# Performance work log

Measured on AMD Instinct MI355X. Metric: run time of the kernel, lower is better.

The kernel has to match this reference:

```python
import jax, jax.numpy as jnp
import numpy as np

N = 50000   # nodes
E = 800000  # edges (avg degree 16)
D = 96      # input feature dim
U = 96      # units (== D, so no dense_i projection)


def _glorot(key, fan_in, fan_out):
    limit = np.sqrt(6.0 / (fan_in + fan_out)).astype(np.float32)
    return jax.random.uniform(key, (fan_in, fan_out), jnp.float32, -limit, limit)


def setup_inputs() -> dict:
    key = jax.random.key(0)
    ks = jax.random.split(key, 8)
    X = jax.random.normal(ks[0], (N, D), jnp.float32)
    row = jax.random.randint(ks[1], (E,), 0, N, jnp.int32)   # destination nodes
    col = jax.random.randint(ks[2], (E,), 0, N, jnp.int32)   # source nodes
    a_vals = jax.random.uniform(ks[3], (E,), jnp.float32)    # adjacency values
    return {
        "X": X,
        "a_vals": a_vals,
        "Wn": _glorot(ks[4], D, U), "bn": jnp.zeros((U,), jnp.float32),
        "Wgi": _glorot(ks[5], D, U), "bgi": jnp.zeros((U,), jnp.float32),
        "Wgn": _glorot(ks[6], U, U), "bgn": jnp.zeros((U,), jnp.float32),
        "row": row, "col": col,
    }


def reference(X, a_vals, Wn, bn, Wgi, bgi, Wgn, bgn, row, col):
    # new_X = dense_n(X); new_X = A @ new_X  (SpMM via gather + segment_sum)
    newX = X @ Wn + bn                       # [N, U]
    msgs = a_vals[:, None] * newX[col]       # [E, U]
    agg = jax.ops.segment_sum(msgs, row, num_segments=N)  # [N, U]
    # gate = sigmoid(dense_gate_i(X) + dense_gate_n(agg))
    gate = jax.nn.sigmoid(X @ Wgi + bgi + agg @ Wgn + bgn)
    # units == inp_dim -> no dense_i; gated residual combine
    return agg * gate + X * (1.0 - gate)
```

## Files before the change

kernel.cpp:

```cpp
#include <hip/hip_runtime.h>
#include <math.h>


#define DU 96
#define DU4 24
#define NSUB 32
#define NGRP 8
#define HMAX 6656
#define CAPG_PAD 16384

typedef unsigned int uint;
typedef unsigned short ushort;
typedef __attribute__((ext_vector_type(8))) short short8;
typedef __attribute__((ext_vector_type(4))) float f32x4;

__device__ inline uint bf16r(float x) {
  uint u = __float_as_uint(x);
  return (u + 0x7FFFu + ((u >> 16) & 1u)) >> 16;
}

__global__ __launch_bounds__(256) void k_fuse1(
    const float* __restrict__ X, const float* __restrict__ Wn,
    const float* __restrict__ bn, const float* __restrict__ Wgi,
    const float* __restrict__ Wgn, const int* __restrict__ row,
    ushort* __restrict__ Xb, ushort* __restrict__ newXb,
    ushort* __restrict__ WTgi, ushort* __restrict__ WTgn,
    ushort* __restrict__ pc, int N, int E, int ntile) {
  __shared__ __align__(16) char smem[31744];
  ushort* WL = (ushort*)smem;
  typedef ushort XsRow[104];
  XsRow* Xs = (XsRow*)(smem + 18432);
  const int tid = threadIdx.x;
  const int lane = tid & 63, w = tid >> 6;
  const int m = lane & 15, q = lane >> 4;

  if ((int)blockIdx.x < ntile) {
    if (blockIdx.x == 0) {
      for (int i = tid; i < DU * DU; i += 256) {
        int n = i / DU, k = i % DU;
        WTgi[i] = (ushort)bf16r(Wgi[k * DU + n]);
      }
    } else if (blockIdx.x == 1) {
      for (int i = tid; i < DU * DU; i += 256) {
        int n = i / DU, k = i % DU;
        WTgn[i] = (ushort)bf16r(Wgn[k * DU + n]);
      }
    }
    for (int idx = tid; idx < 9216; idx += 256) {
      int j = idx & 7, ln = (idx >> 3) & 63, tk = idx >> 9;
      int ks = tk / 6, t = tk % 6;
      int k = ks * 32 + (ln >> 4) * 8 + j;
      int n = t * 16 + (ln & 15);
      WL[idx] = (ushort)bf16r(Wn[k * DU + n]);
    }
    const int row0 = blockIdx.x * 64;
    for (int i = tid; i < 64 * 48; i += 256) {
      int r = i / 48, cu = i % 48;
      int gr = row0 + r;
      uint packed = 0;
      if (gr < N) {
        float2 v = ((const float2*)X)[(size_t)gr * 48 + cu];
        packed = bf16r(v.x) | (bf16r(v.y) << 16);
        ((uint*)Xb)[(size_t)gr * 48 + cu] = packed;
      }
      *(uint*)&Xs[r][cu * 2] = packed;
    }
    __syncthreads();

    f32x4 acc[6];
#pragma unroll
    for (int t = 0; t < 6; ++t) acc[t] = (f32x4){0.f, 0.f, 0.f, 0.f};
#pragma unroll
    for (int ks = 0; ks < 3; ++ks) {
      short8 af = *(const short8*)&Xs[w * 16 + m][ks * 32 + q * 8];
#pragma unroll
      for (int t = 0; t < 6; ++t) {
        short8 bf = *(const short8*)&WL[((ks * 6 + t) * 64 + lane) * 8];
        acc[t] = __builtin_amdgcn_mfma_f32_16x16x32_bf16(af, bf, acc[t], 0, 0, 0);
      }
    }
    __syncthreads();
#pragma unroll
    for (int t = 0; t < 6; ++t) {
      int c = t * 16 + m;
      float bb = bn[c];
#pragma unroll
      for (int i = 0; i < 4; ++i)
        Xs[w * 16 + q * 4 + i][c] = (ushort)bf16r(acc[t][i] + bb);
    }
    __syncthreads();
    for (int i = tid; i < 64 * 48; i += 256) {
      int r = i / 48, cu = i % 48;
      int gr = row0 + r;
      if (gr < N) ((uint*)newXb)[(size_t)gr * 48 + cu] = *(uint*)&Xs[r][cu * 2];
    }
  } else {
    int* hist = (int*)smem;
    const int hb = (int)blockIdx.x - ntile;
    const int g = (int)(blockIdx.x & 7);
    const int sub = hb >> 3;
    const int d0 = (int)((long long)N * g >> 3);
    const int d1 = (int)((long long)N * (g + 1) >> 3);
    const int hs = d1 - d0;
    for (int j = tid; j < hs; j += 256) hist[j] = 0;
    __syncthreads();
    const int e0 = (int)(((long long)E * sub) / NSUB);
    const int e1 = (int)(((long long)E * (sub + 1)) / NSUB);
    int i = e0 + tid;
    for (; i + 1792 < e1; i += 2048) {
      int a0 = row[i], a1 = row[i + 256], a2 = row[i + 512], a3 = row[i + 768];
      int a4 = row[i + 1024], a5 = row[i + 1280], a6 = row[i + 1536], a7 = row[i + 1792];
      if (a0 >= d0 && a0 < d1) atomicAdd(&hist[a0 - d0], 1);
      if (a1 >= d0 && a1 < d1) atomicAdd(&hist[a1 - d0], 1);
      if (a2 >= d0 && a2 < d1) atomicAdd(&hist[a2 - d0], 1);
      if (a3 >= d0 && a3 < d1) atomicAdd(&hist[a3 - d0], 1);
      if (a4 >= d0 && a4 < d1) atomicAdd(&hist[a4 - d0], 1);
      if (a5 >= d0 && a5 < d1) atomicAdd(&hist[a5 - d0], 1);
      if (a6 >= d0 && a6 < d1) atomicAdd(&hist[a6 - d0], 1);
      if (a7 >= d0 && a7 < d1) atomicAdd(&hist[a7 - d0], 1);
    }
    for (; i < e1; i += 256) {
      int d = row[i];
      if (d >= d0 && d < d1) atomicAdd(&hist[d - d0], 1);
    }
    __syncthreads();
    for (int j = tid; j < hs; j += 256) pc[(size_t)sub * N + d0 + j] = (ushort)hist[j];
  }
}

__global__ __launch_bounds__(1024) void k_prep(const ushort* __restrict__ pc,
                                               ushort* __restrict__ psub,
                                               ushort* __restrict__ deg,
                                               int* __restrict__ off,
                                               int N, int E) {
  __shared__ ushort degs[HMAX];
  __shared__ int ws[16];
  const int g = blockIdx.x;
  const int tid = threadIdx.x;
  const int lane = tid & 63, wid = tid >> 6;
  const int d0 = (int)((long long)N * g >> 3);
  const int d1 = (int)((long long)N * (g + 1) >> 3);
  const int hs = d1 - d0;
  for (int j2 = tid * 2; j2 < hs; j2 += 2048) {
    int d2 = d0 + j2;
    int runLo = 0, runHi = 0;
#pragma unroll 8
    for (int s = 0; s < NSUB; ++s) {
      uint v = *(const uint*)(pc + (size_t)s * N + d2);
      *(uint*)(psub + (size_t)s * N + d2) = (uint)runLo | ((uint)runHi << 16);
      runLo += (int)(v & 0xFFFFu);
      runHi += (int)(v >> 16);
    }
    uint dpair = (uint)runLo | ((uint)runHi << 16);
    *(uint*)&degs[j2] = dpair;
    *(uint*)(deg + d2) = dpair;
  }
  __syncthreads();
  const int PT = 8;
  const int j0 = tid * PT;
  int v[PT];
  int s = 0;
#pragma unroll
  for (int k = 0; k < PT; ++k) {
    int j = j0 + k;
    v[k] = (j < hs) ? (int)degs[j] : 0;
    s += v[k];
  }
  int incl = s;
#pragma unroll
  for (int dlt = 1; dlt < 64; dlt <<= 1) {
    int t = __shfl_up(incl, dlt, 64);
    if (lane >= dlt) incl += t;
  }
  if (lane == 63) ws[wid] = incl;
  __syncthreads();
  int wexcl = 0;
#pragma unroll
  for (int k = 0; k < 16; ++k)
    if (k < wid) wexcl += ws[k];
  const int capg = (E >> 3) + CAPG_PAD;
  int running = g * capg + wexcl + (incl - s);
#pragma unroll
  for (int k = 0; k < PT; ++k) {
    int j = j0 + k;
    if (j < hs) { off[d0 + j] = running; running += v[k]; }
  }
}

__global__ __launch_bounds__(256) void k_scatter(const int* __restrict__ row,
                                                 const int* __restrict__ col,
                                                 const float* __restrict__ a_vals,
                                                 const int* __restrict__ off,
                                                 const ushort* __restrict__ psub,
                                                 int2* __restrict__ ec,
                                                 int N, int E) {
  __shared__ int cur[HMAX];
  const int g = (int)(blockIdx.x & 7);
  const int sub = (int)(blockIdx.x >> 3);
  const int d0 = (int)((long long)N * g >> 3);
  const int d1 = (int)((long long)N * (g + 1) >> 3);
  const int hs = d1 - d0;
  for (int j = threadIdx.x; j < hs; j += 256)
    cur[j] = off[d0 + j] + (int)psub[(size_t)sub * N + d0 + j];
  __syncthreads();
  const int e0 = (int)(((long long)E * sub) / NSUB);
  const int e1 = (int)(((long long)E * (sub + 1)) / NSUB);
  int i = e0 + (int)threadIdx.x;
  for (; i + 1792 < e1; i += 2048) {
    int a0 = row[i], a1 = row[i + 256], a2 = row[i + 512], a3 = row[i + 768];
    int a4 = row[i + 1024], a5 = row[i + 1280], a6 = row[i + 1536], a7 = row[i + 1792];
    if (a0 >= d0 && a0 < d1) {
      int s = atomicAdd(&cur[a0 - d0], 1);
      ec[s] = make_int2(col[i], __float_as_int(a_vals[i]));
    }
    if (a1 >= d0 && a1 < d1) {
      int s = atomicAdd(&cur[a1 - d0], 1);
      ec[s] = make_int2(col[i + 256], __float_as_int(a_vals[i + 256]));
    }
    if (a2 >= d0 && a2 < d1) {
      int s = atomicAdd(&cur[a2 - d0], 1);
      ec[s] = make_int2(col[i + 512], __float_as_int(a_vals[i + 512]));
    }
    if (a3 >= d0 && a3 < d1) {
      int s = atomicAdd(&cur[a3 - d0], 1);
      ec[s] = make_int2(col[i + 768], __float_as_int(a_vals[i + 768]));
    }
    if (a4 >= d0 && a4 < d1) {
      int s = atomicAdd(&cur[a4 - d0], 1);
      ec[s] = make_int2(col[i + 1024], __float_as_int(a_vals[i + 1024]));
    }
    if (a5 >= d0 && a5 < d1) {
      int s = atomicAdd(&cur[a5 - d0], 1);
      ec[s] = make_int2(col[i + 1280], __float_as_int(a_vals[i + 1280]));
    }
    if (a6 >= d0 && a6 < d1) {
      int s = atomicAdd(&cur[a6 - d0], 1);
      ec[s] = make_int2(col[i + 1536], __float_as_int(a_vals[i + 1536]));
    }
    if (a7 >= d0 && a7 < d1) {
      int s = atomicAdd(&cur[a7 - d0], 1);
      ec[s] = make_int2(col[i + 1792], __float_as_int(a_vals[i + 1792]));
    }
  }
  for (; i < e1; i += 256) {
    int d = row[i];
    if (d >= d0 && d < d1) {
      int s = atomicAdd(&cur[d - d0], 1);
      ec[s] = make_int2(col[i], __float_as_int(a_vals[i]));
    }
  }
}

__global__ __launch_bounds__(256) void k_aggGate(
    const ushort* __restrict__ Xb, const ushort* __restrict__ newXb,
    const int* __restrict__ off, const ushort* __restrict__ deg,
    const int2* __restrict__ ec, const ushort* __restrict__ WTgi,
    const ushort* __restrict__ WTgn, const float* __restrict__ bgi,
    const float* __restrict__ bgn, const float* __restrict__ X,
    float* __restrict__ Out, int N) {
  __shared__ float As[64][104];
  __shared__ float Gs[64][100];
  const int tid = threadIdx.x;
  const int lane = tid & 63, w = tid >> 6;
  const int m = lane & 15, q = lane >> 4;
  const int row0 = blockIdx.x * 64;

#define GCN_FMA8(ACC, V, A)                                      \
  ACC[0] = fmaf(A, __uint_as_float(V.x << 16), ACC[0]);          \
  ACC[1] = fmaf(A, __uint_as_float(V.x & 0xFFFF0000u), ACC[1]);  \
  ACC[2] = fmaf(A, __uint_as_float(V.y << 16), ACC[2]);          \
  ACC[3] = fmaf(A, __uint_as_float(V.y & 0xFFFF0000u), ACC[3]);  \
  ACC[4] = fmaf(A, __uint_as_float(V.z << 16), ACC[4]);          \
  ACC[5] = fmaf(A, __uint_as_float(V.z & 0xFFFF0000u), ACC[5]);  \
  ACC[6] = fmaf(A, __uint_as_float(V.w << 16), ACC[6]);          \
  ACC[7] = fmaf(A, __uint_as_float(V.w & 0xFFFF0000u), ACC[7])
  for (int t = tid; t < 64 * 12; t += 256) {
    const int rl = t / 12, c = t % 12;
    const int r = row0 + rl;
    float accA[8], accB[8];
#pragma unroll
    for (int k = 0; k < 8; ++k) { accA[k] = 0.f; accB[k] = 0.f; }
    if (r < N) {
      const int2* ep = ec + off[r];
      const int e1 = (int)deg[r];
      int e = 0;
      for (; e + 8 <= e1; e += 8) {
        int2 p0 = ep[e + 0];
        int2 p1 = ep[e + 1];
        int2 p2 = ep[e + 2];
        int2 p3 = ep[e + 3];
        int2 p4 = ep[e + 4];
        int2 p5 = ep[e + 5];
        int2 p6 = ep[e + 6];
        int2 p7 = ep[e + 7];
        uint4 v0 = *(const uint4*)(newXb + (size_t)p0.x * DU + c * 8);
        uint4 v1 = *(const uint4*)(newXb + (size_t)p1.x * DU + c * 8);
        uint4 v2 = *(const uint4*)(newXb + (size_t)p2.x * DU + c * 8);
        uint4 v3 = *(const uint4*)(newXb + (size_t)p3.x * DU + c * 8);
        uint4 v4 = *(const uint4*)(newXb + (size_t)p4.x * DU + c * 8);
        uint4 v5 = *(const uint4*)(newXb + (size_t)p5.x * DU + c * 8);
        uint4 v6 = *(const uint4*)(newXb + (size_t)p6.x * DU + c * 8);
        uint4 v7 = *(const uint4*)(newXb + (size_t)p7.x * DU + c * 8);
        float a0 = __int_as_float(p0.y), a1 = __int_as_float(p1.y);
        float a2 = __int_as_float(p2.y), a3 = __int_as_float(p3.y);
        float a4 = __int_as_float(p4.y), a5 = __int_as_float(p5.y);
        float a6 = __int_as_float(p6.y), a7 = __int_as_float(p7.y);
        GCN_FMA8(accA, v0, a0);
        GCN_FMA8(accB, v1, a1);
        GCN_FMA8(accA, v2, a2);
        GCN_FMA8(accB, v3, a3);
        GCN_FMA8(accA, v4, a4);
        GCN_FMA8(accB, v5, a5);
        GCN_FMA8(accA, v6, a6);
        GCN_FMA8(accB, v7, a7);
      }
      for (; e + 4 <= e1; e += 4) {
        int2 p0 = ep[e + 0];
        int2 p1 = ep[e + 1];
        int2 p2 = ep[e + 2];
        int2 p3 = ep[e + 3];
        uint4 v0 = *(const uint4*)(newXb + (size_t)p0.x * DU + c * 8);
        uint4 v1 = *(const uint4*)(newXb + (size_t)p1.x * DU + c * 8);
        uint4 v2 = *(const uint4*)(newXb + (size_t)p2.x * DU + c * 8);
        uint4 v3 = *(const uint4*)(newXb + (size_t)p3.x * DU + c * 8);
        float a0 = __int_as_float(p0.y), a1 = __int_as_float(p1.y);
        float a2 = __int_as_float(p2.y), a3 = __int_as_float(p3.y);
        GCN_FMA8(accA, v0, a0);
        GCN_FMA8(accB, v1, a1);
        GCN_FMA8(accA, v2, a2);
        GCN_FMA8(accB, v3, a3);
      }
      for (; e < e1; ++e) {
        int2 p = ep[e];
        uint4 v = *(const uint4*)(newXb + (size_t)p.x * DU + c * 8);
        float a = __int_as_float(p.y);
        GCN_FMA8(accA, v, a);
      }
    }
#pragma unroll
    for (int k = 0; k < 8; ++k) accA[k] += accB[k];
    *(float4*)&As[rl][c * 8 + 0] = make_float4(accA[0], accA[1], accA[2], accA[3]);
    *(float4*)&As[rl][c * 8 + 4] = make_float4(accA[4], accA[5], accA[6], accA[7]);
  }
#undef GCN_FMA8
  __syncthreads();

  int ar = row0 + w * 16 + m;
  if (ar > N - 1) ar = N - 1;
  f32x4 acc[6];
#pragma unroll
  for (int t = 0; t < 6; ++t) acc[t] = (f32x4){0.f, 0.f, 0.f, 0.f};
#pragma unroll
  for (int ks = 0; ks < 3; ++ks) {
    short8 af = *(const short8*)(Xb + (size_t)ar * DU + ks * 32 + q * 8);
#pragma unroll
    for (int t = 0; t < 6; ++t) {
      short8 bf = *(const short8*)(WTgi + (size_t)(t * 16 + m) * DU + ks * 32 + q * 8);
      acc[t] = __builtin_amdgcn_mfma_f32_16x16x32_bf16(af, bf, acc[t], 0, 0, 0);
    }
  }
  const int rl = w * 16 + m;
#pragma unroll
  for (int ks = 0; ks < 3; ++ks) {
    float4 u0 = *(const float4*)&As[rl][ks * 32 + q * 8];
    float4 u1 = *(const float4*)&As[rl][ks * 32 + q * 8 + 4];
    short8 af;
    af[0] = (short)bf16r(u0.x); af[1] = (short)bf16r(u0.y);
    af[2] = (short)bf16r(u0.z); af[3] = (short)bf16r(u0.w);
    af[4] = (short)bf16r(u1.x); af[5] = (short)bf16r(u1.y);
    af[6] = (short)bf16r(u1.z); af[7] = (short)bf16r(u1.w);
#pragma unroll
    for (int t = 0; t < 6; ++t) {
      short8 bf = *(const short8*)(WTgn + (size_t)(t * 16 + m) * DU + ks * 32 + q * 8);
      acc[t] = __builtin_amdgcn_mfma_f32_16x16x32_bf16(af, bf, acc[t], 0, 0, 0);
    }
  }
#pragma unroll
  for (int t = 0; t < 6; ++t) {
    int c = t * 16 + m;
    float bb = bgi[c] + bgn[c];
#pragma unroll
    for (int i = 0; i < 4; ++i) {
      float z = acc[t][i] + bb;
      Gs[w * 16 + q * 4 + i][c] = 1.f / (1.f + __expf(-z));
    }
  }
  __syncthreads();

  for (int j = tid; j < 64 * DU4; j += 256) {
    int r = j / DU4, c = j % DU4;
    int gr = row0 + r;
    if (gr < N) {
      float4 xv = ((const float4*)X)[(size_t)gr * DU4 + c];
      float4 av = *(const float4*)&As[r][c * 4];
      const float* gp = &Gs[r][c * 4];
      float4 o;
      o.x = xv.x + gp[0] * (av.x - xv.x);
      o.y = xv.y + gp[1] * (av.y - xv.y);
      o.z = xv.z + gp[2] * (av.z - xv.z);
      o.w = xv.w + gp[3] * (av.w - xv.w);
      ((float4*)Out)[(size_t)gr * DU4 + c] = o;
    }
  }
}

extern "C" void kernel_launch(void* const* d_in, const int* in_sizes, int n_in,
                              void* d_out, int out_size, void* d_ws, size_t ws_size,
                              hipStream_t stream) {
  const float* X      = (const float*)d_in[0];
  const float* a_vals = (const float*)d_in[1];
  const float* Wn     = (const float*)d_in[2];
  const float* bn     = (const float*)d_in[3];
  const float* Wgi    = (const float*)d_in[4];
  const float* bgi    = (const float*)d_in[5];
  const float* Wgn    = (const float*)d_in[6];
  const float* bgn    = (const float*)d_in[7];
  const int*   row    = (const int*)d_in[8];
  const int*   col    = (const int*)d_in[9];
  float* out = (float*)d_out;

  const int N = in_sizes[0] / DU;
  const int E = in_sizes[1];
  const int ntile = (N + 63) / 64;
  const int G1 = ntile + NSUB * NGRP;
  const int capg = (E >> 3) + CAPG_PAD;

  int2*   ec    = (int2*)d_ws;
  ushort* Xb    = (ushort*)(ec + (size_t)NGRP * capg);
  ushort* newXb = Xb + (size_t)N * DU;
  ushort* WTgi  = newXb + (size_t)N * DU;
  ushort* WTgn  = WTgi + DU * DU;
  int*    off   = (int*)(WTgn + DU * DU);
  ushort* deg   = (ushort*)(off + ((N + 3) & ~3));
  ushort* pc    = deg + (((size_t)N + 7) & ~7ull);
  ushort* psub  = pc + (size_t)NSUB * N;

  k_fuse1  <<<G1, 256, 0, stream>>>(X, Wn, bn, Wgi, Wgn, row,
                                    Xb, newXb, WTgi, WTgn, pc, N, E, ntile);
  k_prep   <<<NGRP, 1024, 0, stream>>>(pc, psub, deg, off, N, E);
  k_scatter<<<NSUB * NGRP, 256, 0, stream>>>(row, col, a_vals, off, psub, ec, N, E);
  k_aggGate<<<ntile, 256, 0, stream>>>(Xb, newXb, off, deg, ec, WTgi, WTgn,
                                       bgi, bgn, X, out, N);
}
```

Baseline: 218.9 us.

## Split prep into parallel colsum and offset kernels, widen scatter, slim aggGate epilogue

Moves the per-node column prefix sum over sub-histograms out of the 8-block prep kernel into a grid-wide kernel, leaving a small offset-scan kernel. Doubles NSUB and uses 512-thread scatter blocks to raise parallelism in histogram and scatter. In aggGate, stores the aggregate as bf16 in shared memory, drops the gate shared buffer and a barrier, fuses both gate GEMM loops, and remaps block indices so consecutive blocks interleave across the 8 edge-storage groups. Risks: extra launch, more psub traffic, and a bf16-rounded aggregate in the output combine instead of fp32, which reduces accuracy.

```diff
diff --git a/kernel.cpp b/kernel.cpp
--- a/kernel.cpp
+++ b/kernel.cpp
@@ -4,7 +4,7 @@
 
 #define DU 96
 #define DU4 24
-#define NSUB 32
+#define NSUB 64
 #define NGRP 8
 #define HMAX 6656
 #define CAPG_PAD 16384
@@ -128,12 +128,25 @@
   }
 }
 
-__global__ __launch_bounds__(1024) void k_prep(const ushort* __restrict__ pc,
-                                               ushort* __restrict__ psub,
-                                               ushort* __restrict__ deg,
-                                               int* __restrict__ off,
-                                               int N, int E) {
-  __shared__ ushort degs[HMAX];
+__global__ __launch_bounds__(256) void k_colsum(const ushort* __restrict__ pc,
+                                                ushort* __restrict__ psub,
+                                                ushort* __restrict__ deg, int N) {
+  int d2 = (blockIdx.x * 256 + threadIdx.x) * 2;
+  if (d2 >= N) return;
+  int runLo = 0, runHi = 0;
+#pragma unroll 8
+  for (int s = 0; s < NSUB; ++s) {
+    uint v = *(const uint*)(pc + (size_t)s * N + d2);
+    *(uint*)(psub + (size_t)s * N + d2) = (uint)runLo | ((uint)runHi << 16);
+    runLo += (int)(v & 0xFFFFu);
+    runHi += (int)(v >> 16);
+  }
+  *(uint*)(deg + d2) = (uint)runLo | ((uint)runHi << 16);
+}
+
+__global__ __launch_bounds__(1024) void k_off(const ushort* __restrict__ deg,
+                                              int* __restrict__ off,
+                                              int N, int E) {
   __shared__ int ws[16];
   const int g = blockIdx.x;
   const int tid = threadIdx.x;
@@ -141,21 +154,6 @@
   const int d0 = (int)((long long)N * g >> 3);
   const int d1 = (int)((long long)N * (g + 1) >> 3);
   const int hs = d1 - d0;
-  for (int j2 = tid * 2; j2 < hs; j2 += 2048) {
-    int d2 = d0 + j2;
-    int runLo = 0, runHi = 0;
-#pragma unroll 8
-    for (int s = 0; s < NSUB; ++s) {
-      uint v = *(const uint*)(pc + (size_t)s * N + d2);
-      *(uint*)(psub + (size_t)s * N + d2) = (uint)runLo | ((uint)runHi << 16);
-      runLo += (int)(v & 0xFFFFu);
-      runHi += (int)(v >> 16);
-    }
-    uint dpair = (uint)runLo | ((uint)runHi << 16);
-    *(uint*)&degs[j2] = dpair;
-    *(uint*)(deg + d2) = dpair;
-  }
-  __syncthreads();
   const int PT = 8;
   const int j0 = tid * PT;
   int v[PT];
@@ -163,7 +161,7 @@
 #pragma unroll
   for (int k = 0; k < PT; ++k) {
     int j = j0 + k;
-    v[k] = (j < hs) ? (int)degs[j] : 0;
+    v[k] = (j < hs) ? (int)deg[d0 + j] : 0;
     s += v[k];
   }
   int incl = s;
@@ -187,7 +185,7 @@
   }
 }
 
-__global__ __launch_bounds__(256) void k_scatter(const int* __restrict__ row,
+__global__ __launch_bounds__(512) void k_scatter(const int* __restrict__ row,
                                                  const int* __restrict__ col,
                                                  const float* __restrict__ a_vals,
                                                  const int* __restrict__ off,
@@ -200,49 +198,49 @@
   const int d0 = (int)((long long)N * g >> 3);
   const int d1 = (int)((long long)N * (g + 1) >> 3);
   const int hs = d1 - d0;
-  for (int j = threadIdx.x; j < hs; j += 256)
+  for (int j = threadIdx.x; j < hs; j += 512)
     cur[j] = off[d0 + j] + (int)psub[(size_t)sub * N + d0 + j];
   __syncthreads();
   const int e0 = (int)(((long long)E * sub) / NSUB);
   const int e1 = (int)(((long long)E * (sub + 1)) / NSUB);
   int i = e0 + (int)threadIdx.x;
-  for (; i + 1792 < e1; i += 2048) {
-    int a0 = row[i], a1 = row[i + 256], a2 = row[i + 512], a3 = row[i + 768];
-    int a4 = row[i + 1024], a5 = row[i + 1280], a6 = row[i + 1536], a7 = row[i + 1792];
+  for (; i + 3584 < e1; i += 4096) {
+    int a0 = row[i], a1 = row[i + 512], a2 = row[i + 1024], a3 = row[i + 1536];
+    int a4 = row[i + 2048], a5 = row[i + 2560], a6 = row[i + 3072], a7 = row[i + 3584];
     if (a0 >= d0 && a0 < d1) {
       int s = atomicAdd(&cur[a0 - d0], 1);
       ec[s] = make_int2(col[i], __float_as_int(a_vals[i]));
     }
     if (a1 >= d0 && a1 < d1) {
       int s = atomicAdd(&cur[a1 - d0], 1);
-      ec[s] = make_int2(col[i + 256], __float_as_int(a_vals[i + 256]));
+      ec[s] = make_int2(col[i + 512], __float_as_int(a_vals[i + 512]));
     }
     if (a2 >= d0 && a2 < d1) {
       int s = atomicAdd(&cur[a2 - d0], 1);
-      ec[s] = make_int2(col[i + 512], __float_as_int(a_vals[i + 512]));
+      ec[s] = make_int2(col[i + 1024], __float_as_int(a_vals[i + 1024]));
     }
     if (a3 >= d0 && a3 < d1) {
       int s = atomicAdd(&cur[a3 - d0], 1);
-      ec[s] = make_int2(col[i + 768], __float_as_int(a_vals[i + 768]));
+      ec[s] = make_int2(col[i + 1536], __float_as_int(a_vals[i + 1536]));
     }
     if (a4 >= d0 && a4 < d1) {
       int s = atomicAdd(&cur[a4 - d0], 1);
-      ec[s] = make_int2(col[i + 1024], __float_as_int(a_vals[i + 1024]));
+      ec[s] = make_int2(col[i + 2048], __float_as_int(a_vals[i + 2048]));
     }
     if (a5 >= d0 && a5 < d1) {
       int s = atomicAdd(&cur[a5 - d0], 1);
-      ec[s] = make_int2(col[i + 1280], __float_as_int(a_vals[i + 1280]));
+      ec[s] = make_int2(col[i + 2560], __float_as_int(a_vals[i + 2560]));
     }
     if (a6 >= d0 && a6 < d1) {
       int s = atomicAdd(&cur[a6 - d0], 1);
-      ec[s] = make_int2(col[i + 1536], __float_as_int(a_vals[i + 1536]));
+      ec[s] = make_int2(col[i + 3072], __float_as_int(a_vals[i + 3072]));
     }
     if (a7 >= d0 && a7 < d1) {
       int s = atomicAdd(&cur[a7 - d0], 1);
-      ec[s] = make_int2(col[i + 1792], __float_as_int(a_vals[i + 1792]));
-    }
-  }
-  for (; i < e1; i += 256) {
+      ec[s] = make_int2(col[i + 3584], __float_as_int(a_vals[i + 3584]));
+    }
+  }
+  for (; i < e1; i += 512) {
     int d = row[i];
     if (d >= d0 && d < d1) {
       int s = atomicAdd(&cur[d - d0], 1);
@@ -257,13 +255,18 @@
     const int2* __restrict__ ec, const ushort* __restrict__ WTgi,
     const ushort* __restrict__ WTgn, const float* __restrict__ bgi,
     const float* __restrict__ bgn, const float* __restrict__ X,
-    float* __restrict__ Out, int N) {
-  __shared__ float As[64][104];
-  __shared__ float Gs[64][100];
+    float* __restrict__ Out, int N, int ntile) {
+  __shared__ ushort As[64][104];
   const int tid = threadIdx.x;
   const int lane = tid & 63, w = tid >> 6;
   const int m = lane & 15, q = lane >> 4;
-  const int row0 = blockIdx.x * 64;
+  const int g = (int)(blockIdx.x & 7);
+  const int j = (int)(blockIdx.x >> 3);
+  const int q0 = ntile >> 3, r0 = ntile & 7;
+  const int sz = q0 + (g < r0 ? 1 : 0);
+  if (j >= sz) return;
+  const int tile = (g < r0 ? g * (q0 + 1) : r0 * (q0 + 1) + (g - r0) * q0) + j;
+  const int row0 = tile * 64;
 
 #define GCN_FMA8(ACC, V, A)                                      \
   ACC[0] = fmaf(A, __uint_as_float(V.x << 16), ACC[0]);          \
@@ -339,8 +342,12 @@
     }
 #pragma unroll
     for (int k = 0; k < 8; ++k) accA[k] += accB[k];
-    *(float4*)&As[rl][c * 8 + 0] = make_float4(accA[0], accA[1], accA[2], accA[3]);
-    *(float4*)&As[rl][c * 8 + 4] = make_float4(accA[4], accA[5], accA[6], accA[7]);
+    uint4 o;
+    o.x = bf16r(accA[0]) | (bf16r(accA[1]) << 16);
+    o.y = bf16r(accA[2]) | (bf16r(accA[3]) << 16);
+    o.z = bf16r(accA[4]) | (bf16r(accA[5]) << 16);
+    o.w = bf16r(accA[6]) | (bf16r(accA[7]) << 16);
+    *(uint4*)&As[rl][c * 8] = o;
   }
 #undef GCN_FMA8
   __syncthreads();
@@ -353,53 +360,31 @@
 #pragma unroll
   for (int ks = 0; ks < 3; ++ks) {
     short8 af = *(const short8*)(Xb + (size_t)ar * DU + ks * 32 + q * 8);
+    short8 ag = *(const short8*)&As[w * 16 + m][ks * 32 + q * 8];
 #pragma unroll
     for (int t = 0; t < 6; ++t) {
       short8 bf = *(const short8*)(WTgi + (size_t)(t * 16 + m) * DU + ks * 32 + q * 8);
       acc[t] = __builtin_amdgcn_mfma_f32_16x16x32_bf16(af, bf, acc[t], 0, 0, 0);
-    }
-  }
-  const int rl = w * 16 + m;
-#pragma unroll
-  for (int ks = 0; ks < 3; ++ks) {
-    float4 u0 = *(const float4*)&As[rl][ks * 32 + q * 8];
-    float4 u1 = *(const float4*)&As[rl][ks * 32 + q * 8 + 4];
-    short8 af;
-    af[0] = (short)bf16r(u0.x); af[1] = (short)bf16r(u0.y);
-    af[2] = (short)bf16r(u0.z); af[3] = (short)bf16r(u0.w);
-    af[4] = (short)bf16r(u1.x); af[5] = (short)bf16r(u1.y);
-    af[6] = (short)bf16r(u1.z); af[7] = (short)bf16r(u1.w);
-#pragma unroll
-    for (int t = 0; t < 6; ++t) {
-      short8 bf = *(const short8*)(WTgn + (size_t)(t * 16 + m) * DU + ks * 32 + q * 8);
-      acc[t] = __builtin_amdgcn_mfma_f32_16x16x32_bf16(af, bf, acc[t], 0, 0, 0);
-    }
-  }
+      short8 bg = *(const short8*)(WTgn + (size_t)(t * 16 + m) * DU + ks * 32 + q * 8);
+      acc[t] = __builtin_amdgcn_mfma_f32_16x16x32_bf16(ag, bg, acc[t], 0, 0, 0);
+    }
+  }
+
 #pragma unroll
   for (int t = 0; t < 6; ++t) {
-    int c = t * 16 + m;
-    float bb = bgi[c] + bgn[c];
+    const int c = t * 16 + m;
+    const float bb = bgi[c] + bgn[c];
 #pragma unroll
     for (int i = 0; i < 4; ++i) {
-      float z = acc[t][i] + bb;
-      Gs[w * 16 + q * 4 + i][c] = 1.f / (1.f + __expf(-z));
-    }
-  }
-  __syncthreads();
-
-  for (int j = tid; j < 64 * DU4; j += 256) {
-    int r = j / DU4, c = j % DU4;
-    int gr = row0 + r;
-    if (gr < N) {
-      float4 xv = ((const float4*)X)[(size_t)gr * DU4 + c];
-      float4 av = *(const float4*)&As[r][c * 4];
-      const float* gp = &Gs[r][c * 4];
-      float4 o;
-      o.x = xv.x + gp[0] * (av.x - xv.x);
-      o.y = xv.y + gp[1] * (av.y - xv.y);
-      o.z = xv.z + gp[2] * (av.z - xv.z);
-      o.w = xv.w + gp[3] * (av.w - xv.w);
-      ((float4*)Out)[(size_t)gr * DU4 + c] = o;
+      const int rl = w * 16 + q * 4 + i;
+      const int gr = row0 + rl;
+      if (gr < N) {
+        float z = acc[t][i] + bb;
+        float gate = 1.f / (1.f + __expf(-z));
+        float xv = X[(size_t)gr * DU + c];
+        float av = __uint_as_float((uint)As[rl][c] << 16);
+        Out[(size_t)gr * DU + c] = xv + gate * (av - xv);
+      }
     }
   }
 }
@@ -437,8 +422,10 @@
 
   k_fuse1  <<<G1, 256, 0, stream>>>(X, Wn, bn, Wgi, Wgn, row,
                                     Xb, newXb, WTgi, WTgn, pc, N, E, ntile);
-  k_prep   <<<NGRP, 1024, 0, stream>>>(pc, psub, deg, off, N, E);
-  k_scatter<<<NSUB * NGRP, 256, 0, stream>>>(row, col, a_vals, off, psub, ec, N, E);
-  k_aggGate<<<ntile, 256, 0, stream>>>(Xb, newXb, off, deg, ec, WTgi, WTgn,
-                                       bgi, bgn, X, out, N);
-}
+  k_colsum <<<(N / 2 + 255) / 256, 256, 0, stream>>>(pc, psub, deg, N);
+  k_off    <<<NGRP, 1024, 0, stream>>>(deg, off, N, E);
+  k_scatter<<<NSUB * NGRP, 512, 0, stream>>>(row, col, a_vals, off, psub, ec, N, E);
+  k_aggGate<<<((ntile + 7) / 8) * 8, 256, 0, stream>>>(Xb, newXb, off, deg, ec,
+                                                       WTgi, WTgn, bgi, bgn,
+                                                       X, out, N, ntile);
+}
```

New measurement: 200.8 us. 8.3% less time.
